# Optimization experiments

Measured on AMD Instinct MI355X. Metric: run time of the kernel, lower is better.

The kernel has to match this reference:

```python
import jax, jax.numpy as jnp
import numpy as np

B, C, N = 8, 256, 4096
S = C // 4  # 64
BN_EPS = 1e-5

def setup_inputs() -> dict:
    key = jax.random.key(0)
    ks = jax.random.split(key, 8)
    scale = lambda fan_in: 1.0 / np.sqrt(fan_in)
    x = jax.random.normal(ks[0], (B, C, N), dtype=jnp.float32)
    W_qk = jax.random.normal(ks[1], (S, C), dtype=jnp.float32) * scale(C)
    W_k2c = jax.random.normal(ks[2], (S, C // 2), dtype=jnp.float32) * scale(C // 2)
    W_v = jax.random.normal(ks[3], (C, C), dtype=jnp.float32) * scale(C)
    b_v = jnp.zeros((C,), dtype=jnp.float32)
    W_t = jax.random.normal(ks[4], (C, C), dtype=jnp.float32) * scale(C)
    b_t = jnp.zeros((C,), dtype=jnp.float32)
    bn_gamma = jnp.ones((C,), dtype=jnp.float32)
    bn_beta = jnp.zeros((C,), dtype=jnp.float32)
    bn_mean = jnp.zeros((C,), dtype=jnp.float32)
    bn_var = jnp.ones((C,), dtype=jnp.float32)
    # random.sample(range(C), S): S distinct channel indices
    idx = jax.random.permutation(ks[5], C)[:S].astype(jnp.int32)
    return {"x": x, "W_qk": W_qk, "W_k2c": W_k2c, "W_v": W_v, "b_v": b_v,
            "W_t": W_t, "b_t": b_t, "bn_gamma": bn_gamma, "bn_beta": bn_beta,
            "bn_mean": bn_mean, "bn_var": bn_var, "idx": idx}

def reference(x, W_qk, W_k2c, W_v, b_v, W_t, b_t,
              bn_gamma, bn_beta, bn_mean, bn_var, idx):
    # q = k projection (tied weights), 1x1 conv == channel matmul
    x_q = jnp.einsum('sc,bcn->bns', W_qk, x)            # [B,N,S]
    x_k = jnp.einsum('sc,bcn->bsn', W_qk, x)            # [B,S,N]
    x_k1 = x[:, idx, :]                                  # random channel gather [B,S,N]
    x_k = jnp.concatenate([x_k, x_k1], axis=1)           # [B,C/2,N]
    x_k = jnp.einsum('sh,bhn->bsn', W_k2c, x_k)          # [B,S,N]
    x_k = jax.nn.softmax(x_k, axis=-2)                   # softmax over channel dim
    x_v = jnp.einsum('oc,bcn->bon', W_v, x) + b_v[None, :, None]  # [B,C,N]
    energy = jnp.einsum('bns,bsm->bnm', x_q, x_k)        # [B,N,N]
    attention = jax.nn.softmax(energy, axis=-1)
    attention = attention / (1e-9 + attention.sum(axis=1, keepdims=True))
    x_r = jnp.einsum('bcn,bnm->bcm', x_v, attention)     # [B,C,N]
    x_r = jnp.einsum('oc,bcm->bom', W_t, x_r) + b_t[None, :, None]
    # BatchNorm1d (inference) + ReLU
    inv = bn_gamma / jnp.sqrt(bn_var + BN_EPS)
    x_r = (x_r - bn_mean[None, :, None]) * inv[None, :, None] + bn_beta[None, :, None]
    x_r = jax.nn.relu(x_r)
    return x + x_r
```

## Files before the change

kernel.cpp:

```cpp
#include <hip/hip_runtime.h>
#include <hip/hip_bf16.h>

#define B_ 8
#define C_ 256
#define N_ 4096
#define S_ 64
#define LOG2E 1.4426950408889634f

typedef __attribute__((ext_vector_type(8))) short short8;
typedef __attribute__((ext_vector_type(4))) float f32x4;

__device__ __forceinline__ short f2b(float f) {
  unsigned u = __float_as_uint(f);
  unsigned r = (u + 0x7FFFu + ((u >> 16) & 1u)) >> 16;
  return (short)(r & 0xFFFFu);
}

__device__ __forceinline__ int cvtpk(float lo, float hi) {
  int r;
  asm("v_cvt_pk_bf16_f32 %0, %1, %2" : "=v"(r) : "v"(lo), "v"(hi));
  return r;
}


__global__ __launch_bounds__(256) void kw_conv(const float* __restrict__ Wv,
    const float* __restrict__ Wt, short* __restrict__ Wvf, short* __restrict__ Wtf) {
  int t = blockIdx.x * 256 + threadIdx.x;
  const float* src = (t < 8192) ? Wv : Wt;
  short* dst = (t < 8192) ? Wvf : Wtf;
  int i = (t & 8191) * 8;
  int o = i >> 8, c0c = i & 255;
  short8 v;
#pragma unroll
  for (int j = 0; j < 8; j++) v[j] = f2b(src[i + j]);
  int lane = (o & 15) + 16 * ((c0c >> 3) & 3);
  size_t off = ((((size_t)(o >> 4)) * 8 + (c0c >> 5)) * 64 + lane) * 8;
  *(short8*)(dst + off) = v;
}

__global__ __launch_bounds__(256) void k1_qk(const float* __restrict__ x,
    const float* __restrict__ Wqk, const float* __restrict__ Wk2c,
    const int* __restrict__ idx, short* __restrict__ Qf, short* __restrict__ Kf,
    short* __restrict__ Xf) {
  int bid = blockIdx.x;
  int b = bid & 7, n0 = (bid >> 3) * 64;
  int tn = threadIdx.x;
  int sg = __builtin_amdgcn_readfirstlane(threadIdx.y);
  const float* xb = x + (size_t)b * C_ * N_ + n0 + tn;
  __shared__ short xls[256][73];
  __shared__ float q_lds[64][65];
  __shared__ float red[4][64];
#pragma unroll 4
  for (int i = 0; i < 64; i++) {
    int c = sg * 64 + i;
    xls[c][tn] = f2b(xb[(size_t)c * N_]);
  }
  float acc[16];
#pragma unroll
  for (int i = 0; i < 16; i++) acc[i] = 0.f;
  for (int c = 0; c < C_; c += 4) {
    float x0 = xb[(size_t)c * N_];
    float x1 = xb[(size_t)(c + 1) * N_];
    float x2 = xb[(size_t)(c + 2) * N_];
    float x3 = xb[(size_t)(c + 3) * N_];
#pragma unroll
    for (int i = 0; i < 16; i++) {
      const float* wr = Wqk + (sg * 16 + i) * C_ + c;
      acc[i] += wr[0] * x0 + wr[1] * x1 + wr[2] * x2 + wr[3] * x3;
    }
  }
#pragma unroll
  for (int i = 0; i < 16; i++) q_lds[sg * 16 + i][tn] = acc[i];
  {
    size_t base = (((size_t)b * 256 + (n0 >> 4) + (tn >> 4)) * 2 + (sg >> 1)) * 64;
    int l0 = (tn & 15) + 16 * ((2 * sg) & 3);
    int l1 = (tn & 15) + 16 * ((2 * sg + 1) & 3);
    short8 o0, o1;
#pragma unroll
    for (int i = 0; i < 8; i++) { o0[i] = f2b(acc[i] * LOG2E); o1[i] = f2b(acc[i + 8] * LOG2E); }
    *(short8*)(Qf + (base + l0) * 8) = o0;
    *(short8*)(Qf + (base + l1) * 8) = o1;
  }
  __syncthreads();
#pragma unroll
  for (int i = 0; i < 8; i++) {
    int run = i * 4 + sg;
    int ntl = run >> 3, ks = run & 7;
    short8 o;
#pragma unroll
    for (int j = 0; j < 8; j++)
      o[j] = xls[ks * 32 + ((tn >> 4) & 3) * 8 + j][ntl * 16 + (tn & 15)];
    size_t off = ((((size_t)b * 256 + (n0 >> 4) + ntl) * 8 + ks) * 64 + tn) * 8;
    *(short8*)(Xf + off) = o;
  }
  float acc2[16];
#pragma unroll
  for (int i = 0; i < 16; i++) acc2[i] = 0.f;
  for (int h = 0; h < 64; h += 4) {
    float q0 = q_lds[h][tn], q1 = q_lds[h + 1][tn];
    float q2 = q_lds[h + 2][tn], q3 = q_lds[h + 3][tn];
#pragma unroll
    for (int i = 0; i < 16; i++) {
      const float* wr = Wk2c + (sg * 16 + i) * 128 + h;
      acc2[i] += wr[0] * q0 + wr[1] * q1 + wr[2] * q2 + wr[3] * q3;
    }
  }
  for (int h = 0; h < 64; h += 4) {
    float g0 = xb[(size_t)idx[h] * N_];
    float g1 = xb[(size_t)idx[h + 1] * N_];
    float g2 = xb[(size_t)idx[h + 2] * N_];
    float g3 = xb[(size_t)idx[h + 3] * N_];
#pragma unroll
    for (int i = 0; i < 16; i++) {
      const float* wr = Wk2c + (sg * 16 + i) * 128 + 64 + h;
      acc2[i] += wr[0] * g0 + wr[1] * g1 + wr[2] * g2 + wr[3] * g3;
    }
  }
  float pm = acc2[0];
#pragma unroll
  for (int i = 1; i < 16; i++) pm = fmaxf(pm, acc2[i]);
  red[sg][tn] = pm;
  __syncthreads();
  float mx = fmaxf(fmaxf(red[0][tn], red[1][tn]), fmaxf(red[2][tn], red[3][tn]));
  float ps = 0.f;
  float ex[16];
#pragma unroll
  for (int i = 0; i < 16; i++) { ex[i] = __expf(acc2[i] - mx); ps += ex[i]; }
  __syncthreads();
  red[sg][tn] = ps;
  __syncthreads();
  float inv = 1.f / (red[0][tn] + red[1][tn] + red[2][tn] + red[3][tn]);
  {
    size_t base = (((size_t)b * 256 + (n0 >> 4) + (tn >> 4)) * 2 + (sg >> 1)) * 64;
    int l0 = (tn & 15) + 16 * ((2 * sg) & 3);
    int l1 = (tn & 15) + 16 * ((2 * sg + 1) & 3);
    short8 o0, o1;
#pragma unroll
    for (int i = 0; i < 8; i++) { o0[i] = f2b(ex[i] * inv); o1[i] = f2b(ex[i + 8] * inv); }
    *(short8*)(Kf + (base + l0) * 8) = o0;
    *(short8*)(Kf + (base + l1) * 8) = o1;
  }
}

__global__ __launch_bounds__(256) void k2_xv(const short* __restrict__ Wvf,
    const float* __restrict__ bv, const short* __restrict__ Xf, short* __restrict__ Vf) {
  int bid = blockIdx.x;
  int b = bid & 7, nblk = bid >> 3;
  int lane = threadIdx.x & 63, w = threadIdx.x >> 6;
  int lr = lane & 15, lg = lane >> 4;
  __shared__ short Vt[64][264];
  f32x4 acc[4][4];
#pragma unroll
  for (int i = 0; i < 4; i++)
#pragma unroll
    for (int j = 0; j < 4; j++) acc[i][j] = {0.f, 0.f, 0.f, 0.f};
#pragma unroll 1
  for (int ks = 0; ks < 8; ks++) {
    short8 bfrag[4];
#pragma unroll
    for (int ns = 0; ns < 4; ns++)
      bfrag[ns] = *(const short8*)(Xf + ((((size_t)b * 256 + nblk * 4 + ns) * 8 + ks) * 64 + lane) * 8);
#pragma unroll
    for (int os = 0; os < 4; os++) {
      short8 af = *(const short8*)(Wvf + ((((size_t)(4 * w + os)) * 8 + ks) * 64 + lane) * 8);
#pragma unroll
      for (int ns = 0; ns < 4; ns++)
        acc[os][ns] = __builtin_amdgcn_mfma_f32_16x16x32_bf16(af, bfrag[ns], acc[os][ns], 0, 0, 0);
    }
  }
#pragma unroll
  for (int os = 0; os < 4; os++) {
    int c0 = w * 64 + os * 16 + lg * 4;
    float b0 = bv[c0], b1 = bv[c0 + 1], b2 = bv[c0 + 2], b3 = bv[c0 + 3];
#pragma unroll
    for (int ns = 0; ns < 4; ns++) {
      int2 pk;
      pk.x = cvtpk(acc[os][ns][0] + b0, acc[os][ns][1] + b1);
      pk.y = cvtpk(acc[os][ns][2] + b2, acc[os][ns][3] + b3);
      *(int2*)(&Vt[ns * 16 + lr][c0]) = pk;
    }
  }
  __syncthreads();
#pragma unroll
  for (int rr = 0; rr < 8; rr++) {
    int run = rr * 256 + threadIdx.x;
    int ksl = run >> 10, ctile = (run >> 6) & 15, ln = run & 63;
    short8 o;
#pragma unroll
    for (int j = 0; j < 8; j++)
      o[j] = Vt[ksl * 32 + ((ln >> 4) & 3) * 8 + j][ctile * 16 + (ln & 15)];
    size_t off = ((((size_t)b * 128 + 2 * nblk + ksl) * 16 + ctile) * 64 + ln) * 8;
    *(short8*)(Vf + off) = o;
  }
}

__global__ __launch_bounds__(512) void k3_rse(const short* __restrict__ Qf,
    const short* __restrict__ Kf, float* __restrict__ inv_rse) {
  int bid = blockIdx.x;
  int b = bid & 7, n0 = (bid >> 3) * 64;
  int tid = threadIdx.x;
  int lane = tid & 63, w = tid >> 6;
  int lr = lane & 15, lg = lane >> 4;
  int wn = w & 3, wm = w >> 2;
  __shared__ float red[8][16];
  const short* Qb = Qf + (size_t)b * 256 * 2 * 512;
  const short* Kb = Kf + (size_t)b * 256 * 2 * 512;
  short8 qf[2];
#pragma unroll
  for (int ks = 0; ks < 2; ks++)
    qf[ks] = *(const short8*)(Qb + ((((size_t)((n0 >> 4) + wn)) * 2 + ks) * 64 + lane) * 8);
  int it0 = wm * 32;
  short8 kc[4][2], kn[4][2];
#pragma unroll
  for (int ms = 0; ms < 4; ms++)
#pragma unroll
    for (int ks = 0; ks < 2; ks++)
      kc[ms][ks] = *(const short8*)(Kb + ((((size_t)(it0 * 4 + ms)) * 2 + ks) * 64 + lane) * 8);
  float rs[4] = {0.f, 0.f, 0.f, 0.f};
#pragma unroll 1
  for (int it = it0; it < it0 + 32; ++it) {
    int itn = (it < it0 + 31) ? it + 1 : it;
#pragma unroll
    for (int ms = 0; ms < 4; ms++)
#pragma unroll
      for (int ks = 0; ks < 2; ks++)
        kn[ms][ks] = *(const short8*)(Kb + ((((size_t)(itn * 4 + ms)) * 2 + ks) * 64 + lane) * 8);
#pragma unroll
    for (int ms = 0; ms < 4; ms++) {
      f32x4 e = {0.f, 0.f, 0.f, 0.f};
#pragma unroll
      for (int ks = 0; ks < 2; ks++)
        e = __builtin_amdgcn_mfma_f32_16x16x32_bf16(qf[ks], kc[ms][ks], e, 0, 0, 0);
#pragma unroll
      for (int r = 0; r < 4; r++) rs[r] += __builtin_amdgcn_exp2f(e[r]);
    }
#pragma unroll
    for (int ms = 0; ms < 4; ms++)
#pragma unroll
      for (int ks = 0; ks < 2; ks++) kc[ms][ks] = kn[ms][ks];
  }
#pragma unroll
  for (int off = 1; off < 16; off <<= 1)
#pragma unroll
    for (int r = 0; r < 4; r++) rs[r] += __shfl_xor(rs[r], off, 64);
  if (lr == 0) {
#pragma unroll
    for (int r = 0; r < 4; r++) red[w][lg * 4 + r] = rs[r];
  }
  __syncthreads();
  if (tid < 64) {
    int ntl = tid >> 4, i = tid & 15;
    inv_rse[(size_t)b * N_ + n0 + ntl * 16 + i] = 1.f / (red[ntl][i] + red[ntl + 4][i]);
  }
}

__global__ __launch_bounds__(512, 4) void k4_att(const short* __restrict__ Qf,
    const short* __restrict__ Kf, const short* __restrict__ Vf,
    const float* __restrict__ inv_rse, const short* __restrict__ Wtf,
    const float* __restrict__ bt, const float* __restrict__ gamma,
    const float* __restrict__ beta, const float* __restrict__ mean,
    const float* __restrict__ var, const float* __restrict__ x,
    float* __restrict__ out) {
  int bid = blockIdx.x;
  int b = bid & 7, mblk = bid >> 3, m0 = mblk * 64;
  int tid = threadIdx.x;
  int lane = tid & 63, w = tid >> 6;
  int lr = lane & 15, lg = lane >> 4;
  __shared__ __align__(16) short attf[2][16][64][8];
  __shared__ float cs_red[8][64];
  const short* Qb = Qf + (size_t)b * 256 * 2 * 512;
  const short* Kb = Kf + (size_t)b * 256 * 2 * 512;
  const short* Vb = Vf + (size_t)b * 128 * 16 * 512;
  const float* irb = inv_rse + (size_t)b * N_;
  short8 kfrag[4][2];
#pragma unroll
  for (int ms = 0; ms < 4; ms++)
#pragma unroll
    for (int ks = 0; ks < 2; ks++)
      kfrag[ms][ks] = *(const short8*)(Kb + ((((size_t)(mblk * 4 + ms)) * 2 + ks) * 64 + lane) * 8);
  f32x4 P[2][4];
#pragma unroll
  for (int i = 0; i < 2; i++)
#pragma unroll
    for (int j = 0; j < 4; j++) P[i][j] = {0.f, 0.f, 0.f, 0.f};
  float csum[4] = {0.f, 0.f, 0.f, 0.f};
  short8 qf[2];
#pragma unroll
  for (int ks = 0; ks < 2; ks++)
    qf[ks] = *(const short8*)(Qb + ((((size_t)w) * 2 + ks) * 64 + lane) * 8);
  int kkw = w >> 1;
  int wln = lr + 16 * (((w & 1) << 1) | (lg >> 1));
  int wjo = (lg & 1) * 4;
  int buf = 0;
#pragma unroll 1
  for (int it2 = 0; it2 < 32; ++it2) {
    f32x4 irv = *(const f32x4*)(irb + it2 * 128 + w * 16 + lg * 4);
    f32x4 e[4];
#pragma unroll
    for (int ms = 0; ms < 4; ms++) {
      f32x4 a = {0.f, 0.f, 0.f, 0.f};
#pragma unroll
      for (int ks = 0; ks < 2; ks++)
        a = __builtin_amdgcn_mfma_f32_16x16x32_bf16(qf[ks], kfrag[ms][ks], a, 0, 0, 0);
      e[ms] = a;
    }
    int itn = (it2 < 31) ? it2 + 1 : it2;
    short8 qn[2];
#pragma unroll
    for (int ks = 0; ks < 2; ks++)
      qn[ks] = *(const short8*)(Qb + ((((size_t)(itn * 8 + w)) * 2 + ks) * 64 + lane) * 8);
#pragma unroll
    for (int ms = 0; ms < 4; ms++) {
      float a0 = __builtin_amdgcn_exp2f(e[ms][0]) * irv[0];
      float a1 = __builtin_amdgcn_exp2f(e[ms][1]) * irv[1];
      float a2 = __builtin_amdgcn_exp2f(e[ms][2]) * irv[2];
      float a3 = __builtin_amdgcn_exp2f(e[ms][3]) * irv[3];
      csum[ms] += (a0 + a1) + (a2 + a3);
      int2 pk;
      pk.x = cvtpk(a0, a1);
      pk.y = cvtpk(a2, a3);
      *(int2*)(&attf[buf][kkw * 4 + ms][wln][wjo]) = pk;
    }
    __syncthreads();
    __builtin_amdgcn_s_setprio(1);
#pragma unroll
    for (int kk = 0; kk < 4; kk++) {
      short8 vfr[2];
#pragma unroll
      for (int cs = 0; cs < 2; cs++)
        vfr[cs] = *(const short8*)(Vb + ((((size_t)(it2 * 4 + kk)) * 16 + w * 2 + cs) * 64 + lane) * 8);
      short8 bfr[4];
#pragma unroll
      for (int ms = 0; ms < 4; ms++)
        bfr[ms] = *(const short8*)(&attf[buf][kk * 4 + ms][lane][0]);
#pragma unroll
      for (int cs = 0; cs < 2; cs++)
#pragma unroll
        for (int ms = 0; ms < 4; ms++)
          P[cs][ms] = __builtin_amdgcn_mfma_f32_16x16x32_bf16(vfr[cs], bfr[ms], P[cs][ms], 0, 0, 0);
    }
    __builtin_amdgcn_s_setprio(0);
#pragma unroll
    for (int ks = 0; ks < 2; ks++) qf[ks] = qn[ks];
    buf ^= 1;
  }
#pragma unroll
  for (int off = 16; off < 64; off <<= 1)
#pragma unroll
    for (int ms = 0; ms < 4; ms++) csum[ms] += __shfl_xor(csum[ms], off, 64);
  if (lg == 0) {
#pragma unroll
    for (int ms = 0; ms < 4; ms++) cs_red[w][ms * 16 + lr] = csum[ms];
  }
  __syncthreads();
  float cinv[4];
#pragma unroll
  for (int ms = 0; ms < 4; ms++) {
    int m = ms * 16 + lr;
    float s = 0.f;
#pragma unroll
    for (int ww = 0; ww < 8; ww++) s += cs_red[ww][m];
    cinv[ms] = 1.f / (1e-9f + s);
  }
  short* Rt = (short*)&attf[0][0][0][0];
#pragma unroll
  for (int cs = 0; cs < 2; cs++) {
    int lt = lr + 16 * (cs * 2 + (lg >> 1));
#pragma unroll
    for (int ms = 0; ms < 4; ms++) {
      int2 pk;
      pk.x = cvtpk(P[cs][ms][0] * cinv[ms], P[cs][ms][1] * cinv[ms]);
      pk.y = cvtpk(P[cs][ms][2] * cinv[ms], P[cs][ms][3] * cinv[ms]);
      *(int2*)(Rt + ((ms * 8 + w) * 512 + lt * 8 + (lg & 1) * 4)) = pk;
    }
  }
  __syncthreads();
  f32x4 acc2[2][4];
#pragma unroll
  for (int i = 0; i < 2; i++)
#pragma unroll
    for (int j = 0; j < 4; j++) acc2[i][j] = {0.f, 0.f, 0.f, 0.f};
#pragma unroll 1
  for (int ks = 0; ks < 8; ks++) {
    short8 bfr2[4];
#pragma unroll
    for (int ms = 0; ms < 4; ms++)
      bfr2[ms] = *(const short8*)(Rt + ((ms * 8 + ks) * 512 + lane * 8));
#pragma unroll
    for (int os = 0; os < 2; os++) {
      short8 af = *(const short8*)(Wtf + ((((size_t)(w * 2 + os)) * 8 + ks) * 64 + lane) * 8);
#pragma unroll
      for (int ms = 0; ms < 4; ms++)
        acc2[os][ms] = __builtin_amdgcn_mfma_f32_16x16x32_bf16(af, bfr2[ms], acc2[os][ms], 0, 0, 0);
    }
  }
  const float* xb = x + (size_t)b * C_ * N_ + m0;
  float* ob = out + (size_t)b * C_ * N_ + m0;
#pragma unroll
  for (int os = 0; os < 2; os++)
#pragma unroll
    for (int r = 0; r < 4; r++) {
      int o = w * 32 + os * 16 + lg * 4 + r;
      float bb = bt[o];
      float iv = gamma[o] * rsqrtf(var[o] + 1e-5f);
      float mn = mean[o], be = beta[o];
#pragma unroll
      for (int ms = 0; ms < 4; ms++) {
        int m = ms * 16 + lr;
        float v = (acc2[os][ms][r] + bb - mn) * iv + be;
        v = fmaxf(v, 0.f);
        ob[(size_t)o * N_ + m] = xb[(size_t)o * N_ + m] + v;
      }
    }
}

extern "C" void kernel_launch(void* const* d_in, const int* in_sizes, int n_in,
                              void* d_out, int out_size, void* d_ws, size_t ws_size,
                              hipStream_t stream) {
  const float* x     = (const float*)d_in[0];
  const float* Wqk   = (const float*)d_in[1];
  const float* Wk2c  = (const float*)d_in[2];
  const float* Wv    = (const float*)d_in[3];
  const float* bv    = (const float*)d_in[4];
  const float* Wt    = (const float*)d_in[5];
  const float* bt    = (const float*)d_in[6];
  const float* gamma = (const float*)d_in[7];
  const float* beta  = (const float*)d_in[8];
  const float* mean  = (const float*)d_in[9];
  const float* var   = (const float*)d_in[10];
  const int*   idx   = (const int*)d_in[11];
  float* out = (float*)d_out;

  char* ws = (char*)d_ws;
  size_t off = 0;
  auto alloc = [&](size_t bytes) -> void* {
    void* p = ws + off;
    off = (off + bytes + 255) & ~(size_t)255;
    return p;
  };
  short* Xf   = (short*)alloc((size_t)B_ * N_ * C_ * 2);
  short* Qf   = (short*)alloc((size_t)B_ * N_ * S_ * 2);
  short* Kf   = (short*)alloc((size_t)B_ * N_ * S_ * 2);
  short* Vf   = (short*)alloc((size_t)B_ * C_ * N_ * 2);
  float* irse = (float*)alloc((size_t)B_ * N_ * 4);
  short* Wvf  = (short*)alloc((size_t)C_ * C_ * 2);
  short* Wtf  = (short*)alloc((size_t)C_ * C_ * 2);

  kw_conv<<<dim3(64), 256, 0, stream>>>(Wv, Wt, Wvf, Wtf);
  k1_qk<<<dim3(512), dim3(64, 4), 0, stream>>>(x, Wqk, Wk2c, idx, Qf, Kf, Xf);
  k2_xv<<<dim3(512), 256, 0, stream>>>(Wvf, bv, Xf, Vf);
  k3_rse<<<dim3(512), 512, 0, stream>>>(Qf, Kf, irse);
  k4_att<<<dim3(512), 512, 0, stream>>>(Qf, Kf, Vf, irse, Wtf,
                                        bt, gamma, beta, mean, var, x, out);
}
```

Measured before the change: 317.7 us.

## Fuse Q and V projections into one MFMA kernel and prefetch V in attention

Merges the Q-projection and V-projection kernels. Both now run as bf16 MFMA from a shared LDS tile of x, so the intermediate Xf buffer and one launch go away. The Q projection moves from scalar fp32 FMAs to bf16 tensor-core math, which may change precision slightly. In the attention kernel, K fragments are staged in LDS instead of registers, and V fragments plus inverse row sums are prefetched one iteration ahead. The occupancy hint drops from 4 to 3 waves to absorb the extra register pressure.

```diff
diff --git a/kernel.cpp b/kernel.cpp
--- a/kernel.cpp
+++ b/kernel.cpp
@@ -24,11 +24,13 @@
 
 
 __global__ __launch_bounds__(256) void kw_conv(const float* __restrict__ Wv,
-    const float* __restrict__ Wt, short* __restrict__ Wvf, short* __restrict__ Wtf) {
+    const float* __restrict__ Wt, const float* __restrict__ Wqk,
+    short* __restrict__ Wvf, short* __restrict__ Wtf, short* __restrict__ Wqkf) {
   int t = blockIdx.x * 256 + threadIdx.x;
-  const float* src = (t < 8192) ? Wv : Wt;
-  short* dst = (t < 8192) ? Wvf : Wtf;
-  int i = (t & 8191) * 8;
+  const float* src; short* dst; int i;
+  if (t < 8192)       { src = Wv;  dst = Wvf;  i = t * 8; }
+  else if (t < 16384) { src = Wt;  dst = Wtf;  i = (t - 8192) * 8; }
+  else                { src = Wqk; dst = Wqkf; i = (t - 16384) * 8; }
   int o = i >> 8, c0c = i & 255;
   short8 v;
 #pragma unroll
@@ -38,60 +40,87 @@
   *(short8*)(dst + off) = v;
 }
 
-__global__ __launch_bounds__(256) void k1_qk(const float* __restrict__ x,
-    const float* __restrict__ Wqk, const float* __restrict__ Wk2c,
+__global__ __launch_bounds__(256) void k12(const float* __restrict__ x,
+    const short* __restrict__ Wqkf, const short* __restrict__ Wvf,
+    const float* __restrict__ Wk2c, const float* __restrict__ bv,
     const int* __restrict__ idx, short* __restrict__ Qf, short* __restrict__ Kf,
-    short* __restrict__ Xf) {
+    short* __restrict__ Vf) {
   int bid = blockIdx.x;
-  int b = bid & 7, n0 = (bid >> 3) * 64;
-  int tn = threadIdx.x;
-  int sg = __builtin_amdgcn_readfirstlane(threadIdx.y);
+  int b = bid & 7, nblk = bid >> 3, n0 = nblk * 64;
+  int tid = threadIdx.x;
+  int tn = tid & 63, sg = tid >> 6;
+  int lane = tn, lr = lane & 15, lg = lane >> 4;
   const float* xb = x + (size_t)b * C_ * N_ + n0 + tn;
-  __shared__ short xls[256][73];
+  __shared__ short xls_raw[256 * 73];
   __shared__ float q_lds[64][65];
   __shared__ float red[4][64];
-#pragma unroll 4
+  auto xls = (short(*)[73])xls_raw;
+#pragma unroll 8
   for (int i = 0; i < 64; i++) {
     int c = sg * 64 + i;
     xls[c][tn] = f2b(xb[(size_t)c * N_]);
   }
-  float acc[16];
-#pragma unroll
-  for (int i = 0; i < 16; i++) acc[i] = 0.f;
-  for (int c = 0; c < C_; c += 4) {
-    float x0 = xb[(size_t)c * N_];
-    float x1 = xb[(size_t)(c + 1) * N_];
-    float x2 = xb[(size_t)(c + 2) * N_];
-    float x3 = xb[(size_t)(c + 3) * N_];
-#pragma unroll
-    for (int i = 0; i < 16; i++) {
-      const float* wr = Wqk + (sg * 16 + i) * C_ + c;
-      acc[i] += wr[0] * x0 + wr[1] * x1 + wr[2] * x2 + wr[3] * x3;
-    }
-  }
-#pragma unroll
-  for (int i = 0; i < 16; i++) q_lds[sg * 16 + i][tn] = acc[i];
-  {
-    size_t base = (((size_t)b * 256 + (n0 >> 4) + (tn >> 4)) * 2 + (sg >> 1)) * 64;
-    int l0 = (tn & 15) + 16 * ((2 * sg) & 3);
-    int l1 = (tn & 15) + 16 * ((2 * sg + 1) & 3);
-    short8 o0, o1;
-#pragma unroll
-    for (int i = 0; i < 8; i++) { o0[i] = f2b(acc[i] * LOG2E); o1[i] = f2b(acc[i + 8] * LOG2E); }
-    *(short8*)(Qf + (base + l0) * 8) = o0;
-    *(short8*)(Qf + (base + l1) * 8) = o1;
-  }
-  __syncthreads();
-#pragma unroll
-  for (int i = 0; i < 8; i++) {
-    int run = i * 4 + sg;
-    int ntl = run >> 3, ks = run & 7;
+  __syncthreads();
+  f32x4 accq[4];
+  f32x4 accv[4][4];
+#pragma unroll
+  for (int i = 0; i < 4; i++) {
+    accq[i] = {0.f, 0.f, 0.f, 0.f};
+#pragma unroll
+    for (int j = 0; j < 4; j++) accv[i][j] = {0.f, 0.f, 0.f, 0.f};
+  }
+#pragma unroll 1
+  for (int ks = 0; ks < 8; ks++) {
+    short8 bfrag[4];
+#pragma unroll
+    for (int nt = 0; nt < 4; nt++) {
+      short8 o;
+#pragma unroll
+      for (int j = 0; j < 8; j++)
+        o[j] = xls[ks * 32 + lg * 8 + j][nt * 16 + lr];
+      bfrag[nt] = o;
+    }
+    short8 aq = *(const short8*)(Wqkf + (((size_t)(sg * 8 + ks)) * 64 + lane) * 8);
+#pragma unroll
+    for (int nt = 0; nt < 4; nt++)
+      accq[nt] = __builtin_amdgcn_mfma_f32_16x16x32_bf16(aq, bfrag[nt], accq[nt], 0, 0, 0);
+#pragma unroll
+    for (int ot = 0; ot < 4; ot++) {
+      short8 av = *(const short8*)(Wvf + ((((size_t)(sg * 4 + ot)) * 8 + ks) * 64 + lane) * 8);
+#pragma unroll
+      for (int nt = 0; nt < 4; nt++)
+        accv[ot][nt] = __builtin_amdgcn_mfma_f32_16x16x32_bf16(av, bfrag[nt], accv[ot][nt], 0, 0, 0);
+    }
+  }
+#pragma unroll
+  for (int nt = 0; nt < 4; nt++)
+#pragma unroll
+    for (int r = 0; r < 4; r++)
+      q_lds[sg * 16 + lg * 4 + r][nt * 16 + lr] = accq[nt][r];
+  __syncthreads();
+  short* Vt = xls_raw;
+#pragma unroll
+  for (int ot = 0; ot < 4; ot++) {
+    int c0 = sg * 64 + ot * 16 + lg * 4;
+    float b0 = bv[c0], b1 = bv[c0 + 1], b2 = bv[c0 + 2], b3 = bv[c0 + 3];
+#pragma unroll
+    for (int nt = 0; nt < 4; nt++) {
+      int2 pk;
+      pk.x = cvtpk(accv[ot][nt][0] + b0, accv[ot][nt][1] + b1);
+      pk.y = cvtpk(accv[ot][nt][2] + b2, accv[ot][nt][3] + b3);
+      *(int2*)(&Vt[(size_t)(nt * 16 + lr) * 264 + c0]) = pk;
+    }
+  }
+#pragma unroll
+  for (int rr = 0; rr < 2; rr++) {
+    int run = rr * 4 + sg;
+    int ntl = run >> 1, ks2 = run & 1;
     short8 o;
 #pragma unroll
     for (int j = 0; j < 8; j++)
-      o[j] = xls[ks * 32 + ((tn >> 4) & 3) * 8 + j][ntl * 16 + (tn & 15)];
-    size_t off = ((((size_t)b * 256 + (n0 >> 4) + ntl) * 8 + ks) * 64 + tn) * 8;
-    *(short8*)(Xf + off) = o;
+      o[j] = f2b(q_lds[ks2 * 32 + lg * 8 + j][ntl * 16 + lr] * LOG2E);
+    size_t off = ((((size_t)b * 256 + nblk * 4 + ntl) * 2 + ks2) * 64 + lane) * 8;
+    *(short8*)(Qf + off) = o;
   }
   float acc2[16];
 #pragma unroll
@@ -131,7 +160,7 @@
   __syncthreads();
   float inv = 1.f / (red[0][tn] + red[1][tn] + red[2][tn] + red[3][tn]);
   {
-    size_t base = (((size_t)b * 256 + (n0 >> 4) + (tn >> 4)) * 2 + (sg >> 1)) * 64;
+    size_t base = (((size_t)b * 256 + nblk * 4 + (tn >> 4)) * 2 + (sg >> 1)) * 64;
     int l0 = (tn & 15) + 16 * ((2 * sg) & 3);
     int l1 = (tn & 15) + 16 * ((2 * sg + 1) & 3);
     short8 o0, o1;
@@ -140,55 +169,14 @@
     *(short8*)(Kf + (base + l0) * 8) = o0;
     *(short8*)(Kf + (base + l1) * 8) = o1;
   }
-}
-
-__global__ __launch_bounds__(256) void k2_xv(const short* __restrict__ Wvf,
-    const float* __restrict__ bv, const short* __restrict__ Xf, short* __restrict__ Vf) {
-  int bid = blockIdx.x;
-  int b = bid & 7, nblk = bid >> 3;
-  int lane = threadIdx.x & 63, w = threadIdx.x >> 6;
-  int lr = lane & 15, lg = lane >> 4;
-  __shared__ short Vt[64][264];
-  f32x4 acc[4][4];
-#pragma unroll
-  for (int i = 0; i < 4; i++)
-#pragma unroll
-    for (int j = 0; j < 4; j++) acc[i][j] = {0.f, 0.f, 0.f, 0.f};
-#pragma unroll 1
-  for (int ks = 0; ks < 8; ks++) {
-    short8 bfrag[4];
-#pragma unroll
-    for (int ns = 0; ns < 4; ns++)
-      bfrag[ns] = *(const short8*)(Xf + ((((size_t)b * 256 + nblk * 4 + ns) * 8 + ks) * 64 + lane) * 8);
-#pragma unroll
-    for (int os = 0; os < 4; os++) {
-      short8 af = *(const short8*)(Wvf + ((((size_t)(4 * w + os)) * 8 + ks) * 64 + lane) * 8);
-#pragma unroll
-      for (int ns = 0; ns < 4; ns++)
-        acc[os][ns] = __builtin_amdgcn_mfma_f32_16x16x32_bf16(af, bfrag[ns], acc[os][ns], 0, 0, 0);
-    }
-  }
-#pragma unroll
-  for (int os = 0; os < 4; os++) {
-    int c0 = w * 64 + os * 16 + lg * 4;
-    float b0 = bv[c0], b1 = bv[c0 + 1], b2 = bv[c0 + 2], b3 = bv[c0 + 3];
-#pragma unroll
-    for (int ns = 0; ns < 4; ns++) {
-      int2 pk;
-      pk.x = cvtpk(acc[os][ns][0] + b0, acc[os][ns][1] + b1);
-      pk.y = cvtpk(acc[os][ns][2] + b2, acc[os][ns][3] + b3);
-      *(int2*)(&Vt[ns * 16 + lr][c0]) = pk;
-    }
-  }
-  __syncthreads();
 #pragma unroll
   for (int rr = 0; rr < 8; rr++) {
-    int run = rr * 256 + threadIdx.x;
+    int run = rr * 256 + tid;
     int ksl = run >> 10, ctile = (run >> 6) & 15, ln = run & 63;
     short8 o;
 #pragma unroll
     for (int j = 0; j < 8; j++)
-      o[j] = Vt[ksl * 32 + ((ln >> 4) & 3) * 8 + j][ctile * 16 + (ln & 15)];
+      o[j] = Vt[(size_t)(ksl * 32 + ((ln >> 4) & 3) * 8 + j) * 264 + ctile * 16 + (ln & 15)];
     size_t off = ((((size_t)b * 128 + 2 * nblk + ksl) * 16 + ctile) * 64 + ln) * 8;
     *(short8*)(Vf + off) = o;
   }
@@ -254,7 +242,7 @@
   }
 }
 
-__global__ __launch_bounds__(512, 4) void k4_att(const short* __restrict__ Qf,
+__global__ __launch_bounds__(512, 3) void k4_att(const short* __restrict__ Qf,
     const short* __restrict__ Kf, const short* __restrict__ Vf,
     const float* __restrict__ inv_rse, const short* __restrict__ Wtf,
     const float* __restrict__ bt, const float* __restrict__ gamma,
@@ -267,17 +255,17 @@
   int lane = tid & 63, w = tid >> 6;
   int lr = lane & 15, lg = lane >> 4;
   __shared__ __align__(16) short attf[2][16][64][8];
+  __shared__ __align__(16) short kst[8 * 64 * 8];
   __shared__ float cs_red[8][64];
   const short* Qb = Qf + (size_t)b * 256 * 2 * 512;
   const short* Kb = Kf + (size_t)b * 256 * 2 * 512;
   const short* Vb = Vf + (size_t)b * 128 * 16 * 512;
   const float* irb = inv_rse + (size_t)b * N_;
-  short8 kfrag[4][2];
-#pragma unroll
-  for (int ms = 0; ms < 4; ms++)
-#pragma unroll
-    for (int ks = 0; ks < 2; ks++)
-      kfrag[ms][ks] = *(const short8*)(Kb + ((((size_t)(mblk * 4 + ms)) * 2 + ks) * 64 + lane) * 8);
+  {
+    int ms = tid >> 7, ks2 = (tid >> 6) & 1, ln = tid & 63;
+    short8 kv = *(const short8*)(Kb + ((((size_t)(mblk * 4 + ms)) * 2 + ks2) * 64 + ln) * 8);
+    *(short8*)(kst + ((ms * 2 + ks2) * 64 + ln) * 8) = kv;
+  }
   f32x4 P[2][4];
 #pragma unroll
   for (int i = 0; i < 2; i++)
@@ -288,27 +276,43 @@
 #pragma unroll
   for (int ks = 0; ks < 2; ks++)
     qf[ks] = *(const short8*)(Qb + ((((size_t)w) * 2 + ks) * 64 + lane) * 8);
+  short8 vf[4][2];
+#pragma unroll
+  for (int kk = 0; kk < 4; kk++)
+#pragma unroll
+    for (int cs = 0; cs < 2; cs++)
+      vf[kk][cs] = *(const short8*)(Vb + ((((size_t)kk) * 16 + w * 2 + cs) * 64 + lane) * 8);
+  f32x4 irv = *(const f32x4*)(irb + w * 16 + lg * 4);
   int kkw = w >> 1;
   int wln = lr + 16 * (((w & 1) << 1) | (lg >> 1));
   int wjo = (lg & 1) * 4;
   int buf = 0;
-#pragma unroll 1
+  __syncthreads();
+#pragma unroll 2
   for (int it2 = 0; it2 < 32; ++it2) {
-    f32x4 irv = *(const f32x4*)(irb + it2 * 128 + w * 16 + lg * 4);
+    int itn = (it2 < 31) ? it2 + 1 : it2;
+    short8 vn[4][2];
+#pragma unroll
+    for (int kk = 0; kk < 4; kk++)
+#pragma unroll
+      for (int cs = 0; cs < 2; cs++)
+        vn[kk][cs] = *(const short8*)(Vb + ((((size_t)(itn * 4 + kk)) * 16 + w * 2 + cs) * 64 + lane) * 8);
+    short8 qn[2];
+#pragma unroll
+    for (int ks = 0; ks < 2; ks++)
+      qn[ks] = *(const short8*)(Qb + ((((size_t)(itn * 8 + w)) * 2 + ks) * 64 + lane) * 8);
+    f32x4 irn = *(const f32x4*)(irb + itn * 128 + w * 16 + lg * 4);
     f32x4 e[4];
 #pragma unroll
     for (int ms = 0; ms < 4; ms++) {
       f32x4 a = {0.f, 0.f, 0.f, 0.f};
 #pragma unroll
-      for (int ks = 0; ks < 2; ks++)
-        a = __builtin_amdgcn_mfma_f32_16x16x32_bf16(qf[ks], kfrag[ms][ks], a, 0, 0, 0);
+      for (int ks = 0; ks < 2; ks++) {
+        short8 kf = *(const short8*)(kst + ((ms * 2 + ks) * 64 + lane) * 8);
+        a = __builtin_amdgcn_mfma_f32_16x16x32_bf16(qf[ks], kf, a, 0, 0, 0);
+      }
       e[ms] = a;
     }
-    int itn = (it2 < 31) ? it2 + 1 : it2;
-    short8 qn[2];
-#pragma unroll
-    for (int ks = 0; ks < 2; ks++)
-      qn[ks] = *(const short8*)(Qb + ((((size_t)(itn * 8 + w)) * 2 + ks) * 64 + lane) * 8);
 #pragma unroll
     for (int ms = 0; ms < 4; ms++) {
       float a0 = __builtin_amdgcn_exp2f(e[ms][0]) * irv[0];
@@ -325,10 +329,6 @@
     __builtin_amdgcn_s_setprio(1);
 #pragma unroll
     for (int kk = 0; kk < 4; kk++) {
-      short8 vfr[2];
-#pragma unroll
-      for (int cs = 0; cs < 2; cs++)
-        vfr[cs] = *(const short8*)(Vb + ((((size_t)(it2 * 4 + kk)) * 16 + w * 2 + cs) * 64 + lane) * 8);
       short8 bfr[4];
 #pragma unroll
       for (int ms = 0; ms < 4; ms++)
@@ -337,11 +337,16 @@
       for (int cs = 0; cs < 2; cs++)
 #pragma unroll
         for (int ms = 0; ms < 4; ms++)
-          P[cs][ms] = __builtin_amdgcn_mfma_f32_16x16x32_bf16(vfr[cs], bfr[ms], P[cs][ms], 0, 0, 0);
+          P[cs][ms] = __builtin_amdgcn_mfma_f32_16x16x32_bf16(vf[kk][cs], bfr[ms], P[cs][ms], 0, 0, 0);
     }
     __builtin_amdgcn_s_setprio(0);
 #pragma unroll
     for (int ks = 0; ks < 2; ks++) qf[ks] = qn[ks];
+#pragma unroll
+    for (int kk = 0; kk < 4; kk++)
+#pragma unroll
+      for (int cs = 0; cs < 2; cs++) vf[kk][cs] = vn[kk][cs];
+    irv = irn;
     buf ^= 1;
   }
 #pragma unroll
@@ -438,17 +443,16 @@
     off = (off + bytes + 255) & ~(size_t)255;
     return p;
   };
-  short* Xf   = (short*)alloc((size_t)B_ * N_ * C_ * 2);
   short* Qf   = (short*)alloc((size_t)B_ * N_ * S_ * 2);
   short* Kf   = (short*)alloc((size_t)B_ * N_ * S_ * 2);
   short* Vf   = (short*)alloc((size_t)B_ * C_ * N_ * 2);
   float* irse = (float*)alloc((size_t)B_ * N_ * 4);
   short* Wvf  = (short*)alloc((size_t)C_ * C_ * 2);
   short* Wtf  = (short*)alloc((size_t)C_ * C_ * 2);
-
-  kw_conv<<<dim3(64), 256, 0, stream>>>(Wv, Wt, Wvf, Wtf);
-  k1_qk<<<dim3(512), dim3(64, 4), 0, stream>>>(x, Wqk, Wk2c, idx, Qf, Kf, Xf);
-  k2_xv<<<dim3(512), 256, 0, stream>>>(Wvf, bv, Xf, Vf);
+  short* Wqkf = (short*)alloc((size_t)S_ * C_ * 2);
+
+  kw_conv<<<dim3(72), 256, 0, stream>>>(Wv, Wt, Wqk, Wvf, Wtf, Wqkf);
+  k12<<<dim3(512), 256, 0, stream>>>(x, Wqkf, Wvf, Wk2c, bv, idx, Qf, Kf, Vf);
   k3_rse<<<dim3(512), 512, 0, stream>>>(Qf, Kf, irse);
   k4_att<<<dim3(512), 512, 0, stream>>>(Qf, Kf, Vf, irse, Wtf,
                                         bt, gamma, beta, mean, var, x, out);
```

New measurement: 279.1 us. 12.2% less time.
